# Kernel tuning notes

Measured on AMD Instinct MI355X. Metric: run time of the kernel, lower is better.

## Reference

```python
import jax, jax.numpy as jnp
import numpy as np

ROPE_BASE = 1000000.0
EPS = 1e-6
N_HEADS = 8


def apply_rope(x, base=ROPE_BASE):
    # x: [b, s, h, d]
    b, s, h, d = x.shape
    half = d // 2
    theta = 1.0 / base ** (2 * jnp.arange(half) / d)          # [half]
    angles = jnp.arange(s)[:, None] * theta[None, :]          # [s, half]
    cos = jnp.cos(angles)[None, :, None, :]                   # [1, s, 1, half]
    sin = jnp.sin(angles)[None, :, None, :]
    x1, x2 = jnp.split(x, 2, axis=-1)
    return jnp.concatenate([x1 * cos - x2 * sin, x1 * sin + x2 * cos], axis=-1)


def setup_inputs() -> dict:
    key = jax.random.key(0)
    ks = jax.random.split(key, 5)
    b, s, dim = 2, 4096, 512
    x = jax.random.normal(ks[0], (b, s, dim), dtype=jnp.float32)
    scale = jnp.ones((dim,), dtype=jnp.float32)
    init = 1.0 / np.sqrt(dim)
    Wq = jax.random.normal(ks[1], (dim, dim), dtype=jnp.float32) * init
    Wk = jax.random.normal(ks[2], (dim, dim), dtype=jnp.float32) * init
    Wv = jax.random.normal(ks[3], (dim, dim), dtype=jnp.float32) * init
    Wo = jax.random.normal(ks[4], (dim, dim), dtype=jnp.float32) * init
    return {"x": x, "scale": scale, "Wq": Wq, "Wk": Wk, "Wv": Wv, "Wo": Wo}


def reference(x, scale, Wq, Wk, Wv, Wo):
    b, s, dim = x.shape
    h = N_HEADS
    dh = dim // h
    # RMSNorm (use_fast_variance=False path)
    variance = jnp.mean(x ** 2, axis=-1, keepdims=True)
    x_norm = x / jnp.sqrt(variance + EPS) * scale
    # Projections (flax Linear: y = x @ kernel, kernel [in, out])
    q = (x_norm @ Wq).reshape(b, s, h, dh)
    k = (x_norm @ Wk).reshape(b, s, h, dh)
    v = (x_norm @ Wv).reshape(b, s, h, dh)
    q = apply_rope(q)
    k = apply_rope(k)
    scores = jnp.einsum('bthd,bshd->bhts', q, k) / jnp.sqrt(jnp.float32(dh))
    mask = jnp.triu(jnp.full((s, s), -jnp.inf, dtype=jnp.float32), k=1)
    scores = scores + mask[None, None, :, :]
    attn = jax.nn.softmax(scores, axis=-1)
    out = jnp.einsum('bhts,bshd->bthd', attn, v).reshape(b, s, dim)
    return out @ Wo
```

## Files before the change

kernel.cpp:

```cpp
#include <hip/hip_runtime.h>
#include <hip/hip_bf16.h>

typedef _Float16 f16;
typedef _Float16 f16x2 __attribute__((ext_vector_type(2)));
typedef _Float16 f16x4 __attribute__((ext_vector_type(4)));
typedef _Float16 f16x8 __attribute__((ext_vector_type(8)));
typedef float f32x4 __attribute__((ext_vector_type(4)));

#define S_LEN 4096
#define DIM   512
#define NH    8
#define DH    64
#define BATCH 2
#define BHDIM (BATCH*NH)

#define QSCALE 0.18033688011112042f

__device__ __forceinline__ void gld16(const f16* g, f16* l) {
#if __has_builtin(__builtin_amdgcn_global_load_lds)
  __builtin_amdgcn_global_load_lds((const __attribute__((address_space(1))) void*)g,
                                   (__attribute__((address_space(3))) void*)l, 16, 0, 0);
#else
  *(f16x8*)l = *(const f16x8*)g;
#endif
}

__device__ __forceinline__ float fexp2(float x) {
#if __has_builtin(__builtin_amdgcn_exp2f)
  return __builtin_amdgcn_exp2f(x);
#else
  return exp2f(x);
#endif
}

__device__ __forceinline__ f16x2 pk2(float a, float b) {
#if __has_builtin(__builtin_amdgcn_cvt_pkrtz)
  auto r = __builtin_amdgcn_cvt_pkrtz(a, b);
  f16x2 o; __builtin_memcpy(&o, &r, sizeof(o));
  return o;
#else
  f16x2 r; r[0] = (f16)a; r[1] = (f16)b; return r;
#endif
}

__global__ __launch_bounds__(256) void prep_kernel(
    const float* __restrict__ x, const float* __restrict__ scale,
    const float* __restrict__ Wq, const float* __restrict__ Wk,
    const float* __restrict__ Wv, const float* __restrict__ Wo,
    f16* __restrict__ xn, f16* __restrict__ wt_qkv, f16* __restrict__ wo_t,
    float* __restrict__ ctab, float* __restrict__ stab) {
  int bid = blockIdx.x;
  int tid = threadIdx.x;
  if (bid < 8192) {
    const float* xr = x + (size_t)bid * DIM;
    float2 v = *(const float2*)(xr + tid*2);
    float ss = v.x*v.x + v.y*v.y;
    #pragma unroll
    for (int off = 32; off > 0; off >>= 1) ss += __shfl_down(ss, off);
    __shared__ float red[4];
    if ((tid & 63) == 0) red[tid >> 6] = ss;
    __syncthreads();
    float tot = red[0] + red[1] + red[2] + red[3];
    float inv = rsqrtf(tot * (1.0f/DIM) + 1e-6f);
    float2 s = *(const float2*)(scale + tid*2);
    xn[(size_t)bid*DIM + tid*2+0] = (f16)(v.x*inv*s.x);
    xn[(size_t)bid*DIM + tid*2+1] = (f16)(v.y*inv*s.y);
  } else if (bid < 9216) {
    __shared__ f16 tile[32][33];
    int b2 = bid - 8192;
    int mat = b2 >> 8;
    int rem = b2 & 255;
    int k0 = (rem >> 4) * 32, n0 = (rem & 15) * 32;
    const float* src = (mat == 0) ? Wq : (mat == 1) ? Wk : (mat == 2) ? Wv : Wo;
    f16* dst = (mat < 3) ? (wt_qkv + (size_t)mat*DIM*DIM) : wo_t;
    int tx = tid & 31, ty = tid >> 5;
    #pragma unroll
    for (int i = 0; i < 32; i += 8)
      tile[ty+i][tx] = (f16)src[(size_t)(k0+ty+i)*DIM + n0+tx];
    __syncthreads();
    #pragma unroll
    for (int i = 0; i < 32; i += 8)
      dst[(size_t)(n0+ty+i)*DIM + k0+tx] = tile[tx][ty+i];
  } else {
    int idx = (bid - 9216)*256 + tid;
    int t = idx >> 5, d = idx & 31;
    float theta = exp2f(-(float)d * (19.931568569324174f / 32.0f));
    float sv, cv;
    sincosf((float)t * theta, &sv, &cv);
    ctab[idx] = cv; stab[idx] = sv;
  }
}

__device__ __forceinline__ void gemm128_acc(
    const f16* __restrict__ A, const f16* __restrict__ Bt,
    int m0, int n0, f16* As, f16* Bs, f32x4 (&acc)[4][4]) {
  const int tid = threadIdx.x;
  const int wave = tid >> 6, lane = tid & 63;
  const int l16 = lane & 15, quad = lane >> 4;
  const int mrow = (wave & 1) * 64, ncol = (wave >> 1) * 64;
  const int srow = tid >> 3;
  const int gc = (tid & 7) ^ ((tid >> 3) & 7);

  for (int k0 = 0; k0 < DIM; k0 += 64) {
    if (k0) __syncthreads();
    #pragma unroll
    for (int i = 0; i < 4; i++) {
      gld16(A  + (size_t)(m0 + i*32 + srow)*DIM + k0 + gc*8, As + i*2048 + tid*8);
      gld16(Bt + (size_t)(n0 + i*32 + srow)*DIM + k0 + gc*8, Bs + i*2048 + tid*8);
    }
    __syncthreads();
    #pragma unroll
    for (int kc = 0; kc < 2; kc++) {
      f16x8 a[4], b[4];
      #pragma unroll
      for (int mt = 0; mt < 4; mt++) {
        int row = mrow + mt*16 + l16;
        a[mt] = *(const f16x8*)(As + row*64 + (((quad + 4*kc) ^ (l16 & 7)) * 8));
      }
      #pragma unroll
      for (int nt = 0; nt < 4; nt++) {
        int row = ncol + nt*16 + l16;
        b[nt] = *(const f16x8*)(Bs + row*64 + (((quad + 4*kc) ^ (l16 & 7)) * 8));
      }
      #pragma unroll
      for (int mt = 0; mt < 4; mt++)
        #pragma unroll
        for (int nt = 0; nt < 4; nt++)
          acc[mt][nt] = __builtin_amdgcn_mfma_f32_16x16x32_f16(a[mt], b[nt], acc[mt][nt], 0, 0, 0);
    }
  }
}

__global__ __launch_bounds__(256) void qkv_gemm_kernel(
    const f16* __restrict__ xn, const f16* __restrict__ wt,
    const float* __restrict__ ctab, const float* __restrict__ stab,
    f16* __restrict__ qbuf, f16* __restrict__ kbuf, f16* __restrict__ vt) {
  __shared__ __align__(16) f16 As[128*64], Bs[128*64];
  int m0 = blockIdx.x * 128, n0 = blockIdx.y * 128;
  f32x4 acc[4][4] = {};
  gemm128_acc(xn, wt, m0, n0, As, Bs, acc);

  const int tid = threadIdx.x;
  const int wave = tid >> 6, lane = tid & 63;
  const int l16 = lane & 15, quad = lane >> 4;
  int ncol = n0 + (wave >> 1) * 64;
  int which = ncol >> 9;
  int head = (ncol >> 6) & 7;
  int mbase = m0 + (wave & 1) * 64;

  if (which <= 1) {
    #pragma unroll
    for (int mt = 0; mt < 4; mt++)
      #pragma unroll
      for (int nt = 0; nt < 2; nt++) {
        int d = nt*16 + l16;
        #pragma unroll
        for (int r = 0; r < 4; r++) {
          int t = (mbase + mt*16 + quad*4 + r) & 4095;
          float cv = ctab[t*32 + d], sv = stab[t*32 + d];
          float x1 = acc[mt][nt][r], x2 = acc[mt][nt+2][r];
          acc[mt][nt][r]   = x1*cv - x2*sv;
          acc[mt][nt+2][r] = x1*sv + x2*cv;
        }
      }
  }
  if (which < 2) {
    float osc = (which == 0) ? QSCALE : 1.0f;
    f16* dst = which ? kbuf : qbuf;
    #pragma unroll
    for (int mt = 0; mt < 4; mt++)
      #pragma unroll
      for (int nt = 0; nt < 4; nt++)
        #pragma unroll
        for (int r = 0; r < 4; r++) {
          int m = mbase + mt*16 + quad*4 + r;
          int b = m >> 12, t = m & 4095;
          dst[(((size_t)(b*NH + head))*S_LEN + t)*DH + nt*16 + l16] = (f16)(acc[mt][nt][r]*osc);
        }
  } else {
    #pragma unroll
    for (int mt = 0; mt < 4; mt++)
      #pragma unroll
      for (int nt = 0; nt < 4; nt++) {
        int m = mbase + mt*16 + quad*4;
        int b = m >> 12, tcol = m & 4095;
        int grp = tcol & ~63;
        int pos = ((mt >> 1)*4 + quad)*8 + (mt & 1)*4;
        int d = nt*16 + l16;
        f16x4 v4 = {(f16)acc[mt][nt][0], (f16)acc[mt][nt][1],
                    (f16)acc[mt][nt][2], (f16)acc[mt][nt][3]};
        *(f16x4*)(vt + ((size_t)((b*NH + head)*DH + d))*S_LEN + grp + pos) = v4;
      }
  }
}

__global__ __launch_bounds__(128, 2) void attn_kernel(
    const f16* __restrict__ qbuf, const f16* __restrict__ kbuf,
    const f16* __restrict__ vtb, f16* __restrict__ ao) {
  int bid = blockIdx.x;
  int bh  = bid & 15;
  int p   = bid >> 4;

  int tid = threadIdx.x;
  int wave = tid >> 6, lane = tid & 63;
  int l16 = lane & 15, quad = lane >> 4;

  const f16* Q = qbuf + (size_t)bh*S_LEN*DH;
  const f16* K = kbuf + (size_t)bh*S_LEN*DH;
  const f16* V = vtb  + (size_t)bh*DH*S_LEN;

  int bandv[2] = {127 - p, p};
  int tcnt[2]  = {((127 - p) >> 1) + 1, (p >> 1) + 1};
  int rbase[2] = {bandv[0]*32 + wave*16, bandv[1]*32 + wave*16};

  f16x8 qa[2][2];
  #pragma unroll
  for (int bi = 0; bi < 2; bi++) {
    const f16* qrow = Q + (size_t)(rbase[bi] + l16)*DH + quad*8;
    qa[bi][0] = *(const f16x8*)(qrow);
    qa[bi][1] = *(const f16x8*)(qrow + 32);
  }

  f32x4 o[2][4] = {};
  float m_i[2] = {-1e30f, -1e30f};
  float l_i[2] = {0.f, 0.f};

  __shared__ __align__(16) f16 kt[2*4096];
  __shared__ __align__(16) f16 vs[2*4096];

  const int gcs = (tid & 7) ^ ((tid >> 3) & 7);
  const int srow = tid >> 3;

  #define STAGE(buf, kv)                                                        \
    do {                                                                        \
      f16* ktb = kt + (buf)*4096;                                               \
      f16* vsb = vs + (buf)*4096;                                               \
      _Pragma("unroll")                                                         \
      for (int n = 0; n < 4; n++) {                                             \
        gld16(K + (size_t)((kv) + n*16 + srow)*DH + gcs*8, ktb + n*1024 + tid*8);\
        gld16(V + (size_t)(n*16 + srow)*S_LEN + (kv) + gcs*8, vsb + n*1024 + tid*8);\
      }                                                                         \
    } while (0)

  STAGE(0, 0);
  __syncthreads();

  int nth = tcnt[0];
  for (int it = 0; it < nth; ++it) {
    int kv0 = it * 64;
    int cur = it & 1;
    if (it + 1 < nth) STAGE(cur ^ 1, kv0 + 64);

    const f16* ktc = kt + cur*4096;
    const f16* vsc = vs + cur*4096;

    bool act1 = (it < tcnt[1]);
    bool dia0 = (it == tcnt[0] - 1), dia1 = (it == tcnt[1] - 1);
    int ntl0 = dia0 ? ((bandv[0] & 1) ? 4 : 2) : 4;
    int ntl1 = act1 ? (dia1 ? ((bandv[1] & 1) ? 4 : 2) : 4) : 0;

    f32x4 st[2][4];
    #pragma unroll
    for (int nt = 0; nt < 4; nt++) {
      bool n0 = (nt < ntl0), n1 = (nt < ntl1);
      if (n0 || n1) {
        int row = nt*16 + l16;
        f16x8 kf0 = *(const f16x8*)(ktc + row*64 + (((quad)     ^ (row & 7))*8));
        f16x8 kf1 = *(const f16x8*)(ktc + row*64 + (((quad + 4) ^ (row & 7))*8));
        if (n0) {
          f32x4 z = {};
          z = __builtin_amdgcn_mfma_f32_16x16x32_f16(kf0, qa[0][0], z, 0, 0, 0);
          st[0][nt] = __builtin_amdgcn_mfma_f32_16x16x32_f16(kf1, qa[0][1], z, 0, 0, 0);
        }
        if (n1) {
          f32x4 z = {};
          z = __builtin_amdgcn_mfma_f32_16x16x32_f16(kf0, qa[1][0], z, 0, 0, 0);
          st[1][nt] = __builtin_amdgcn_mfma_f32_16x16x32_f16(kf1, qa[1][1], z, 0, 0, 0);
        }
      }
    }

    f16x8 pa[2][2];
    #pragma unroll
    for (int bi = 0; bi < 2; bi++) {
      int ntl = bi ? ntl1 : ntl0;
      if (ntl == 0) continue;
      bool diag = bi ? dia1 : dia0;
      int qglob = rbase[bi] + l16;
      float rmx = -1e30f;
      #pragma unroll
      for (int nt = 0; nt < 4; nt++) {
        if (nt >= ntl) continue;
        if (diag) {
          int kb = kv0 + nt*16 + quad*4;
          #pragma unroll
          for (int r = 0; r < 4; r++) {
            float v = st[bi][nt][r];
            if (kb + r > qglob) v = -1e30f;
            st[bi][nt][r] = v;
            rmx = fmaxf(rmx, v);
          }
        } else {
          #pragma unroll
          for (int r = 0; r < 4; r++) rmx = fmaxf(rmx, st[bi][nt][r]);
        }
      }
      rmx = fmaxf(rmx, __shfl_xor(rmx, 16));
      rmx = fmaxf(rmx, __shfl_xor(rmx, 32));
      if (!__all(rmx <= m_i[bi] + 8.0f)) {
        float mnew = fmaxf(m_i[bi], rmx);
        float alpha = fexp2(m_i[bi] - mnew);
        m_i[bi] = mnew;
        float al[4];
        #pragma unroll
        for (int r = 0; r < 4; r++) al[r] = __shfl(alpha, quad*4 + r);
        #pragma unroll
        for (int dnt = 0; dnt < 4; dnt++)
          #pragma unroll
          for (int r = 0; r < 4; r++) o[bi][dnt][r] *= al[r];
        l_i[bi] *= alpha;
      }
      float mref = m_i[bi];
      int kcl = ntl >> 1;
      float rs = 0.f;
      #pragma unroll
      for (int c = 0; c < 2; c++) {
        if (c >= kcl) continue;
        float e0 = fexp2(st[bi][2*c  ][0] - mref);
        float e1 = fexp2(st[bi][2*c  ][1] - mref);
        float e2 = fexp2(st[bi][2*c  ][2] - mref);
        float e3 = fexp2(st[bi][2*c  ][3] - mref);
        float e4 = fexp2(st[bi][2*c+1][0] - mref);
        float e5 = fexp2(st[bi][2*c+1][1] - mref);
        float e6 = fexp2(st[bi][2*c+1][2] - mref);
        float e7 = fexp2(st[bi][2*c+1][3] - mref);
        rs += ((e0+e1)+(e2+e3)) + ((e4+e5)+(e6+e7));
        f16x4 h0 = __builtin_shufflevector(pk2(e0,e1), pk2(e2,e3), 0,1,2,3);
        f16x4 h1 = __builtin_shufflevector(pk2(e4,e5), pk2(e6,e7), 0,1,2,3);
        pa[bi][c] = __builtin_shufflevector(h0, h1, 0,1,2,3,4,5,6,7);
      }
      l_i[bi] += rs;
    }

    int kcl0 = ntl0 >> 1, kcl1 = ntl1 >> 1;
    #pragma unroll
    for (int c = 0; c < 2; c++) {
      bool lv0 = (c < kcl0), lv1 = (c < kcl1);
      if (!lv0 && !lv1) continue;
      #pragma unroll
      for (int dnt = 0; dnt < 4; dnt++) {
        int vr = dnt*16 + l16;
        f16x8 vf = *(const f16x8*)(vsc + vr*64 + (((c*4 + quad) ^ (vr & 7))*8));
        if (lv0) o[0][dnt] = __builtin_amdgcn_mfma_f32_16x16x32_f16(pa[0][c], vf, o[0][dnt], 0, 0, 0);
        if (lv1) o[1][dnt] = __builtin_amdgcn_mfma_f32_16x16x32_f16(pa[1][c], vf, o[1][dnt], 0, 0, 0);
      }
    }

    __syncthreads();
  }
  #undef STAGE

  int b = bh >> 3, h = bh & 7;
  #pragma unroll
  for (int bi = 0; bi < 2; bi++) {
    float lf = l_i[bi];
    lf += __shfl_xor(lf, 16);
    lf += __shfl_xor(lf, 32);
    float lr[4];
    #pragma unroll
    for (int r = 0; r < 4; r++) lr[r] = __shfl(lf, quad*4 + r);
    #pragma unroll
    for (int r = 0; r < 4; r++) {
      float invl = 1.0f / lr[r];
      int t = rbase[bi] + quad*4 + r;
      size_t rowoff = ((size_t)(b*S_LEN + t))*DIM + h*DH;
      #pragma unroll
      for (int dnt = 0; dnt < 4; dnt++)
        ao[rowoff + dnt*16 + l16] = (f16)(o[bi][dnt][r]*invl);
    }
  }
}

__global__ __launch_bounds__(256) void out_gemm_kernel(
    const f16* __restrict__ ao, const f16* __restrict__ wot,
    float* __restrict__ out) {
  __shared__ __align__(16) f16 As[128*64], Bs[128*64];
  int m0 = blockIdx.x * 128, n0 = blockIdx.y * 128;
  f32x4 acc[4][4] = {};
  gemm128_acc(ao, wot, m0, n0, As, Bs, acc);

  const int tid = threadIdx.x;
  const int wave = tid >> 6, lane = tid & 63;
  const int l16 = lane & 15, quad = lane >> 4;
  int ncol = n0 + (wave >> 1) * 64;
  int mbase = m0 + (wave & 1) * 64;
  #pragma unroll
  for (int mt = 0; mt < 4; mt++)
    #pragma unroll
    for (int nt = 0; nt < 4; nt++)
      #pragma unroll
      for (int r = 0; r < 4; r++)
        out[(size_t)(mbase + mt*16 + quad*4 + r)*DIM + ncol + nt*16 + l16] = acc[mt][nt][r];
}

extern "C" void kernel_launch(void* const* d_in, const int* in_sizes, int n_in,
                              void* d_out, int out_size, void* d_ws, size_t ws_size,
                              hipStream_t stream) {
  const float* x     = (const float*)d_in[0];
  const float* scale = (const float*)d_in[1];
  const float* Wq    = (const float*)d_in[2];
  const float* Wk    = (const float*)d_in[3];
  const float* Wv    = (const float*)d_in[4];
  const float* Wo    = (const float*)d_in[5];
  float* out = (float*)d_out;

  const size_t ROWS = (size_t)BATCH * S_LEN;
  char* ws = (char*)d_ws;
  f16* xn     = (f16*)ws;  ws += ROWS * DIM * sizeof(f16);
  f16* wt_qkv = (f16*)ws;  ws += (size_t)3 * DIM * DIM * sizeof(f16);
  f16* wo_t   = (f16*)ws;  ws += (size_t)DIM * DIM * sizeof(f16);
  f16* qb     = (f16*)ws;  ws += (size_t)BHDIM * S_LEN * DH * sizeof(f16);
  f16* kb     = (f16*)ws;  ws += (size_t)BHDIM * S_LEN * DH * sizeof(f16);
  f16* vt     = (f16*)ws;  ws += (size_t)BHDIM * S_LEN * DH * sizeof(f16);
  float* ctab = (float*)ws; ws += (size_t)S_LEN * 32 * sizeof(float);
  float* stab = (float*)ws; ws += (size_t)S_LEN * 32 * sizeof(float);
  f16* ao     = xn;

  size_t need = (size_t)(ws - (char*)d_ws);
  if (ws_size < need) return;

  prep_kernel    <<<9728, 256, 0, stream>>>(x, scale, Wq, Wk, Wv, Wo,
                                            xn, wt_qkv, wo_t, ctab, stab);
  qkv_gemm_kernel<<<dim3(64,12), 256, 0, stream>>>(xn, wt_qkv, ctab, stab, qb, kb, vt);
  attn_kernel    <<<1024, 128, 0, stream>>>(qb, kb, vt, ao);
  out_gemm_kernel<<<dim3(64,4), 256, 0, stream>>>(ao, wo_t, out);
}
```

Before: 200.5 us.

## Split attention query bands across separate waves with 256-thread blocks

The attention kernel now runs 4 waves per block instead of 2. Each pair of waves handles one of the two paired query bands, rather than every wave processing both bands. This cuts per-wave register pressure and serial MFMA/softmax work, and staging uses twice as many threads. The cost is that waves on the short band go idle for most iterations while still hitting the barrier each iteration.

Measured after the change: 192.6 us. -4.0%, faster.

```diff
diff --git a/kernel.cpp b/kernel.cpp
--- a/kernel.cpp
+++ b/kernel.cpp
@@ -194,7 +194,7 @@
   }
 }
 
-__global__ __launch_bounds__(128, 2) void attn_kernel(
+__global__ __launch_bounds__(256, 4) void attn_kernel(
     const f16* __restrict__ qbuf, const f16* __restrict__ kbuf,
     const f16* __restrict__ vtb, f16* __restrict__ ao) {
   int bid = blockIdx.x;
@@ -204,48 +204,48 @@
   int tid = threadIdx.x;
   int wave = tid >> 6, lane = tid & 63;
   int l16 = lane & 15, quad = lane >> 4;
+  int bi = wave >> 1, half = wave & 1;
 
   const f16* Q = qbuf + (size_t)bh*S_LEN*DH;
   const f16* K = kbuf + (size_t)bh*S_LEN*DH;
   const f16* V = vtb  + (size_t)bh*DH*S_LEN;
 
-  int bandv[2] = {127 - p, p};
-  int tcnt[2]  = {((127 - p) >> 1) + 1, (p >> 1) + 1};
-  int rbase[2] = {bandv[0]*32 + wave*16, bandv[1]*32 + wave*16};
-
-  f16x8 qa[2][2];
-  #pragma unroll
-  for (int bi = 0; bi < 2; bi++) {
-    const f16* qrow = Q + (size_t)(rbase[bi] + l16)*DH + quad*8;
-    qa[bi][0] = *(const f16x8*)(qrow);
-    qa[bi][1] = *(const f16x8*)(qrow + 32);
-  }
-
-  f32x4 o[2][4] = {};
-  float m_i[2] = {-1e30f, -1e30f};
-  float l_i[2] = {0.f, 0.f};
+  int bv = bi ? p : (127 - p);
+  int tc = (bv >> 1) + 1;
+  int nth = ((127 - p) >> 1) + 1;
+  int rbase = bv*32 + half*16;
+
+  f16x8 qa0, qa1;
+  {
+    const f16* qrow = Q + (size_t)(rbase + l16)*DH + quad*8;
+    qa0 = *(const f16x8*)(qrow);
+    qa1 = *(const f16x8*)(qrow + 32);
+  }
+
+  f32x4 o[4] = {};
+  float m_i = -1e30f;
+  float l_i = 0.f;
 
   __shared__ __align__(16) f16 kt[2*4096];
   __shared__ __align__(16) f16 vs[2*4096];
 
-  const int gcs = (tid & 7) ^ ((tid >> 3) & 7);
   const int srow = tid >> 3;
+  const int gcs = (tid & 7) ^ (srow & 7);
 
   #define STAGE(buf, kv)                                                        \
     do {                                                                        \
       f16* ktb = kt + (buf)*4096;                                               \
       f16* vsb = vs + (buf)*4096;                                               \
       _Pragma("unroll")                                                         \
-      for (int n = 0; n < 4; n++) {                                             \
-        gld16(K + (size_t)((kv) + n*16 + srow)*DH + gcs*8, ktb + n*1024 + tid*8);\
-        gld16(V + (size_t)(n*16 + srow)*S_LEN + (kv) + gcs*8, vsb + n*1024 + tid*8);\
+      for (int n = 0; n < 2; n++) {                                             \
+        gld16(K + (size_t)((kv) + n*32 + srow)*DH + gcs*8, ktb + n*2048 + tid*8);\
+        gld16(V + (size_t)(n*32 + srow)*S_LEN + (kv) + gcs*8, vsb + n*2048 + tid*8);\
       }                                                                         \
     } while (0)
 
   STAGE(0, 0);
   __syncthreads();
 
-  int nth = tcnt[0];
   for (int it = 0; it < nth; ++it) {
     int kv0 = it * 64;
     int cur = it & 1;
@@ -254,39 +254,24 @@
     const f16* ktc = kt + cur*4096;
     const f16* vsc = vs + cur*4096;
 
-    bool act1 = (it < tcnt[1]);
-    bool dia0 = (it == tcnt[0] - 1), dia1 = (it == tcnt[1] - 1);
-    int ntl0 = dia0 ? ((bandv[0] & 1) ? 4 : 2) : 4;
-    int ntl1 = act1 ? (dia1 ? ((bandv[1] & 1) ? 4 : 2) : 4) : 0;
-
-    f32x4 st[2][4];
-    #pragma unroll
-    for (int nt = 0; nt < 4; nt++) {
-      bool n0 = (nt < ntl0), n1 = (nt < ntl1);
-      if (n0 || n1) {
+    if (it < tc) {
+      bool diag = (it == tc - 1);
+      int ntl = diag ? ((bv & 1) ? 4 : 2) : 4;
+      int kcl = ntl >> 1;
+
+      f32x4 st[4];
+      #pragma unroll
+      for (int nt = 0; nt < 4; nt++) {
+        if (nt >= ntl) continue;
         int row = nt*16 + l16;
         f16x8 kf0 = *(const f16x8*)(ktc + row*64 + (((quad)     ^ (row & 7))*8));
         f16x8 kf1 = *(const f16x8*)(ktc + row*64 + (((quad + 4) ^ (row & 7))*8));
-        if (n0) {
-          f32x4 z = {};
-          z = __builtin_amdgcn_mfma_f32_16x16x32_f16(kf0, qa[0][0], z, 0, 0, 0);
-          st[0][nt] = __builtin_amdgcn_mfma_f32_16x16x32_f16(kf1, qa[0][1], z, 0, 0, 0);
-        }
-        if (n1) {
-          f32x4 z = {};
-          z = __builtin_amdgcn_mfma_f32_16x16x32_f16(kf0, qa[1][0], z, 0, 0, 0);
-          st[1][nt] = __builtin_amdgcn_mfma_f32_16x16x32_f16(kf1, qa[1][1], z, 0, 0, 0);
-        }
-      }
-    }
-
-    f16x8 pa[2][2];
-    #pragma unroll
-    for (int bi = 0; bi < 2; bi++) {
-      int ntl = bi ? ntl1 : ntl0;
-      if (ntl == 0) continue;
-      bool diag = bi ? dia1 : dia0;
-      int qglob = rbase[bi] + l16;
+        f32x4 z = {};
+        z = __builtin_amdgcn_mfma_f32_16x16x32_f16(kf0, qa0, z, 0, 0, 0);
+        st[nt] = __builtin_amdgcn_mfma_f32_16x16x32_f16(kf1, qa1, z, 0, 0, 0);
+      }
+
+      int qglob = rbase + l16;
       float rmx = -1e30f;
       #pragma unroll
       for (int nt = 0; nt < 4; nt++) {
@@ -295,75 +280,71 @@
           int kb = kv0 + nt*16 + quad*4;
           #pragma unroll
           for (int r = 0; r < 4; r++) {
-            float v = st[bi][nt][r];
+            float v = st[nt][r];
             if (kb + r > qglob) v = -1e30f;
-            st[bi][nt][r] = v;
+            st[nt][r] = v;
             rmx = fmaxf(rmx, v);
           }
         } else {
           #pragma unroll
-          for (int r = 0; r < 4; r++) rmx = fmaxf(rmx, st[bi][nt][r]);
+          for (int r = 0; r < 4; r++) rmx = fmaxf(rmx, st[nt][r]);
         }
       }
       rmx = fmaxf(rmx, __shfl_xor(rmx, 16));
       rmx = fmaxf(rmx, __shfl_xor(rmx, 32));
-      if (!__all(rmx <= m_i[bi] + 8.0f)) {
-        float mnew = fmaxf(m_i[bi], rmx);
-        float alpha = fexp2(m_i[bi] - mnew);
-        m_i[bi] = mnew;
+      if (!__all(rmx <= m_i + 8.0f)) {
+        float mnew = fmaxf(m_i, rmx);
+        float alpha = fexp2(m_i - mnew);
+        m_i = mnew;
         float al[4];
         #pragma unroll
         for (int r = 0; r < 4; r++) al[r] = __shfl(alpha, quad*4 + r);
         #pragma unroll
         for (int dnt = 0; dnt < 4; dnt++)
           #pragma unroll
-          for (int r = 0; r < 4; r++) o[bi][dnt][r] *= al[r];
-        l_i[bi] *= alpha;
-      }
-      float mref = m_i[bi];
-      int kcl = ntl >> 1;
+          for (int r = 0; r < 4; r++) o[dnt][r] *= al[r];
+        l_i *= alpha;
+      }
+      float mref = m_i;
       float rs = 0.f;
+      f16x8 pa[2];
       #pragma unroll
       for (int c = 0; c < 2; c++) {
         if (c >= kcl) continue;
-        float e0 = fexp2(st[bi][2*c  ][0] - mref);
-        float e1 = fexp2(st[bi][2*c  ][1] - mref);
-        float e2 = fexp2(st[bi][2*c  ][2] - mref);
-        float e3 = fexp2(st[bi][2*c  ][3] - mref);
-        float e4 = fexp2(st[bi][2*c+1][0] - mref);
-        float e5 = fexp2(st[bi][2*c+1][1] - mref);
-        float e6 = fexp2(st[bi][2*c+1][2] - mref);
-        float e7 = fexp2(st[bi][2*c+1][3] - mref);
+        float e0 = fexp2(st[2*c  ][0] - mref);
+        float e1 = fexp2(st[2*c  ][1] - mref);
+        float e2 = fexp2(st[2*c  ][2] - mref);
+        float e3 = fexp2(st[2*c  ][3] - mref);
+        float e4 = fexp2(st[2*c+1][0] - mref);
+        float e5 = fexp2(st[2*c+1][1] - mref);
+        float e6 = fexp2(st[2*c+1][2] - mref);
+        float e7 = fexp2(st[2*c+1][3] - mref);
         rs += ((e0+e1)+(e2+e3)) + ((e4+e5)+(e6+e7));
         f16x4 h0 = __builtin_shufflevector(pk2(e0,e1), pk2(e2,e3), 0,1,2,3);
         f16x4 h1 = __builtin_shufflevector(pk2(e4,e5), pk2(e6,e7), 0,1,2,3);
-        pa[bi][c] = __builtin_shufflevector(h0, h1, 0,1,2,3,4,5,6,7);
-      }
-      l_i[bi] += rs;
+        pa[c] = __builtin_shufflevector(h0, h1, 0,1,2,3,4,5,6,7);
+      }
+      l_i += rs;
+
+      #pragma unroll
+      for (int c = 0; c < 2; c++) {
+        if (c >= kcl) continue;
+        #pragma unroll
+        for (int dnt = 0; dnt < 4; dnt++) {
+          int vr = dnt*16 + l16;
+          f16x8 vf = *(const f16x8*)(vsc + vr*64 + (((c*4 + quad) ^ (vr & 7))*8));
+          o[dnt] = __builtin_amdgcn_mfma_f32_16x16x32_f16(pa[c], vf, o[dnt], 0, 0, 0);
+        }
+      }
     }
 
-    int kcl0 = ntl0 >> 1, kcl1 = ntl1 >> 1;
-    #pragma unroll
-    for (int c = 0; c < 2; c++) {
-      bool lv0 = (c < kcl0), lv1 = (c < kcl1);
-      if (!lv0 && !lv1) continue;
-      #pragma unroll
-      for (int dnt = 0; dnt < 4; dnt++) {
-        int vr = dnt*16 + l16;
-        f16x8 vf = *(const f16x8*)(vsc + vr*64 + (((c*4 + quad) ^ (vr & 7))*8));
-        if (lv0) o[0][dnt] = __builtin_amdgcn_mfma_f32_16x16x32_f16(pa[0][c], vf, o[0][dnt], 0, 0, 0);
-        if (lv1) o[1][dnt] = __builtin_amdgcn_mfma_f32_16x16x32_f16(pa[1][c], vf, o[1][dnt], 0, 0, 0);
-      }
-    }
-
     __syncthreads();
   }
   #undef STAGE
 
   int b = bh >> 3, h = bh & 7;
-  #pragma unroll
-  for (int bi = 0; bi < 2; bi++) {
-    float lf = l_i[bi];
+  {
+    float lf = l_i;
     lf += __shfl_xor(lf, 16);
     lf += __shfl_xor(lf, 32);
     float lr[4];
@@ -372,11 +353,11 @@
     #pragma unroll
     for (int r = 0; r < 4; r++) {
       float invl = 1.0f / lr[r];
-      int t = rbase[bi] + quad*4 + r;
+      int t = rbase + quad*4 + r;
       size_t rowoff = ((size_t)(b*S_LEN + t))*DIM + h*DH;
       #pragma unroll
       for (int dnt = 0; dnt < 4; dnt++)
-        ao[rowoff + dnt*16 + l16] = (f16)(o[bi][dnt][r]*invl);
+        ao[rowoff + dnt*16 + l16] = (f16)(o[dnt][r]*invl);
     }
   }
 }
@@ -432,6 +413,6 @@
   prep_kernel    <<<9728, 256, 0, stream>>>(x, scale, Wq, Wk, Wv, Wo,
                                             xn, wt_qkv, wo_t, ctab, stab);
   qkv_gemm_kernel<<<dim3(64,12), 256, 0, stream>>>(xn, wt_qkv, ctab, stab, qb, kb, vt);
-  attn_kernel    <<<1024, 128, 0, stream>>>(qb, kb, vt, ao);
+  attn_kernel    <<<1024, 256, 0, stream>>>(qb, kb, vt, ao);
   out_gemm_kernel<<<dim3(64,4), 256, 0, stream>>>(ao, wo_t, out);
 }
```
